# Kernel optimization log

Hardware: AMD Instinct MI355X
Metric: run time of the kernel (lower is better)

The kernel has to match this reference:

```python
import jax, jax.numpy as jnp
import numpy as np

CHUNK = 2048  # row tile size; keeps the [CHUNK, M] tile ~268 MB


def setup_inputs() -> dict:
    key = jax.random.key(0)
    k1, k2, k3 = jax.random.split(key, 3)
    N, M, D = 32768, 32768, 32
    ls = jax.random.uniform(k1, (1,), dtype=jnp.float32, minval=0.1, maxval=1.0)
    x = jax.random.normal(k2, (N, D), dtype=jnp.float32)
    y = jax.random.normal(k3, (M, D), dtype=jnp.float32)
    return {"ls": ls, "x": x, "y": y}


def reference(ls, x, y):
    # out[i] = sum_j exp(-ls * ||x_i - y_j||^2), computed in row tiles
    # (never materializes the full N x M matrix, like KeOps Genred).
    N, D = x.shape
    y_sq = jnp.sum(y * y, axis=1)  # [M]

    def row_chunk(xc):
        # xc: [CHUNK, D]
        x_sq = jnp.sum(xc * xc, axis=1)  # [CHUNK]
        sq = x_sq[:, None] + y_sq[None, :] - 2.0 * (xc @ y.T)  # [CHUNK, M]
        return jnp.sum(jnp.exp(-ls[0] * sq), axis=1)  # [CHUNK]

    x_tiles = x.reshape(N // CHUNK, CHUNK, D)
    out = jax.lax.map(row_chunk, x_tiles)  # [N//CHUNK, CHUNK]
    return out.reshape(N, 1)
```

## Files before the change

### kernel.cpp

```cpp
#include <hip/hip_runtime.h>
#include <math.h>

#define DIM 32
#define BLK 256
#define JSPLIT 16
#define RI   4
#define ITPB (4*RI)
#define GTT  16

typedef _Float16 half8 __attribute__((ext_vector_type(8)));
typedef float    f32x4 __attribute__((ext_vector_type(4)));
typedef float    f32x2 __attribute__((ext_vector_type(2)));

struct hl16 { half8 h; half8 l; };


__global__ __launch_bounds__(BLK) void rbf_prep(
    const float* __restrict__ lsp, const float* __restrict__ x,
    const float* __restrict__ y, int n, int m,
    double* __restrict__ acc, double* __restrict__ scale,
    float* __restrict__ bf, hl16* __restrict__ xhl, hl16* __restrict__ yhl)
{
    int i = blockIdx.x * BLK + threadIdx.x;
    const double c2 = -(double)lsp[0] * 1.4426950408889634074;
    const float mf = (float)(-2.0 * c2);
    if (i < n) {
        const float* xp = x + (size_t)i * DIM;
        double xs = 0.0;
        #pragma unroll
        for (int d = 0; d < DIM; ++d) { double v = (double)xp[d]; xs = fma(v, v, xs); }
        acc[i] = 0.0;
        scale[i] = exp2(c2 * xs);
        const int it = i >> 4, r15 = i & 15;
        #pragma unroll
        for (int q = 0; q < 4; ++q) {
            half8 hh, hl;
            #pragma unroll
            for (int d = 0; d < 8; ++d) {
                float v = xp[q * 8 + d] * mf;
                _Float16 h = (_Float16)v;
                hh[d] = h;
                hl[d] = (_Float16)((v - (float)h) * 4096.0f);
            }
            xhl[it * 64 + q * 16 + r15].h = hh;
            xhl[it * 64 + q * 16 + r15].l = hl;
        }
    }
    if (i < m) {
        const float* yp = y + (size_t)i * DIM;
        double ys = 0.0;
        #pragma unroll
        for (int d = 0; d < DIM; ++d) { double v = (double)yp[d]; ys = fma(v, v, ys); }
        bf[i] = (float)(c2 * ys);
        const int it = i >> 4, r15 = i & 15;
        #pragma unroll
        for (int q = 0; q < 4; ++q) {
            half8 hh, hl;
            #pragma unroll
            for (int d = 0; d < 8; ++d) {
                float v = yp[q * 8 + d];
                _Float16 h = (_Float16)v;
                hh[d] = h;
                hl[d] = (_Float16)((v - (float)h) * 4096.0f);
            }
            yhl[it * 64 + q * 16 + r15].h = hh;
            yhl[it * 64 + q * 16 + r15].l = hl;
        }
    }
}

__global__ __launch_bounds__(BLK, 4) void rbf_main(
    const hl16* __restrict__ xhl, const hl16* __restrict__ yhl,
    const float* __restrict__ bf, double* __restrict__ acc, int chunk_j)
{
    const int lane = threadIdx.x & 63;
    const int wave = threadIdx.x >> 6;
    const int itbase = blockIdx.x * ITPB + wave * RI;
    const int c15 = lane & 15;

    half8 ah[RI], al[RI];
    #pragma unroll
    for (int r = 0; r < RI; ++r) {
        ah[r] = xhl[(itbase + r) * 64 + lane].h;
        al[r] = xhl[(itbase + r) * 64 + lane].l;
    }

    const int jt0 = (blockIdx.y * chunk_j) >> 4;
    const int njt = chunk_j >> 4;

    const f32x4 zq = {0.0f, 0.0f, 0.0f, 0.0f};
    const float k12 = 0x1p-12f;

    double accd[RI][4];
    #pragma unroll
    for (int r = 0; r < RI; ++r)
        #pragma unroll
        for (int e = 0; e < 4; ++e) accd[r][e] = 0.0;

    half8 bh[2], bl[2];
    float bfv[2];
    bh[0] = yhl[(size_t)jt0 * 64 + lane].h;
    bl[0] = yhl[(size_t)jt0 * 64 + lane].l;
    bfv[0] = bf[jt0 * 16 + c15];

    for (int g = 0; g < njt / GTT; ++g) {
        f32x2 accf[RI][2];
        #pragma unroll
        for (int r = 0; r < RI; ++r) {
            accf[r][0] = (f32x2){0.0f, 0.0f};
            accf[r][1] = (f32x2){0.0f, 0.0f};
        }

        #pragma unroll
        for (int tt = 0; tt < GTT; ++tt) {
            const int cur = tt & 1, nxt = cur ^ 1;
            const int jt = jt0 + g * GTT + tt;
            int jn = jt + 1; if (jn >= jt0 + njt) jn = jt0;
            const hl16* __restrict__ yt = yhl + (size_t)jn * 64;
            bh[nxt] = yt[lane].h;
            bl[nxt] = yt[lane].l;
            bfv[nxt] = (bf + jn * 16)[c15];

            f32x2 bf2 = {bfv[cur], bfv[cur]};
            #pragma unroll
            for (int r = 0; r < RI; ++r) {
                f32x4 cm = __builtin_amdgcn_mfma_f32_16x16x32_f16(ah[r], bh[cur], zq, 0, 0, 0);
                f32x4 cl = __builtin_amdgcn_mfma_f32_16x16x32_f16(ah[r], bl[cur], zq, 0, 0, 0);
                cl = __builtin_amdgcn_mfma_f32_16x16x32_f16(al[r], bh[cur], cl, 0, 0, 0);
                f32x2 f0 = {cm[0], cm[1]}, f1 = {cm[2], cm[3]};
                f32x2 l0 = {cl[0], cl[1]}, l1 = {cl[2], cl[3]};
                f0 = l0 * k12 + f0;
                f1 = l1 * k12 + f1;
                f0 = f0 + bf2;
                f1 = f1 + bf2;
                f32x2 e0 = {__builtin_amdgcn_exp2f(f0.x), __builtin_amdgcn_exp2f(f0.y)};
                f32x2 e1 = {__builtin_amdgcn_exp2f(f1.x), __builtin_amdgcn_exp2f(f1.y)};
                accf[r][0] += e0;
                accf[r][1] += e1;
            }
        }
        #pragma unroll
        for (int r = 0; r < RI; ++r) {
            accd[r][0] += (double)accf[r][0].x;
            accd[r][1] += (double)accf[r][0].y;
            accd[r][2] += (double)accf[r][1].x;
            accd[r][3] += (double)accf[r][1].y;
        }
    }

    #pragma unroll
    for (int r = 0; r < RI; ++r) {
        #pragma unroll
        for (int e = 0; e < 4; ++e) {
            double v = accd[r][e];
            v += __shfl_xor(v, 1, 64);
            v += __shfl_xor(v, 2, 64);
            v += __shfl_xor(v, 4, 64);
            v += __shfl_xor(v, 8, 64);
            if (c15 == 0) {
                int row = (itbase + r) * 16 + (lane >> 4) * 4 + e;
                atomicAdd(&acc[row], v);
            }
        }
    }
}

__global__ __launch_bounds__(BLK) void rbf_finish(
    const double* __restrict__ acc, const double* __restrict__ scale,
    float* __restrict__ out, int n)
{
    int i = blockIdx.x * BLK + threadIdx.x;
    if (i < n) out[i] = (float)(acc[i] * scale[i]);
}

extern "C" void kernel_launch(void* const* d_in, const int* in_sizes, int n_in,
                              void* d_out, int out_size, void* d_ws, size_t ws_size,
                              hipStream_t stream)
{
    const float* ls = (const float*)d_in[0];
    const float* x  = (const float*)d_in[1];
    const float* y  = (const float*)d_in[2];
    const int n = in_sizes[1] / DIM;
    const int m = in_sizes[2] / DIM;
    float* out = (float*)d_out;

    char* ws = (char*)d_ws;
    double* acc   = (double*)ws;
    double* scale = acc + n;
    float*  bf    = (float*)(scale + n);
    hl16*   xhl   = (hl16*)(bf + m);
    hl16*   yhl   = xhl + (size_t)(n / 16) * 64;

    const int nm = (n > m) ? n : m;
    rbf_prep<<<(nm + BLK - 1) / BLK, BLK, 0, stream>>>(
        ls, x, y, n, m, acc, scale, bf, xhl, yhl);

    const int chunk = m / JSPLIT;
    dim3 grid(n / (16 * ITPB), JSPLIT);
    rbf_main<<<grid, BLK, 0, stream>>>(xhl, yhl, bf, acc, chunk);

    rbf_finish<<<(n + BLK - 1) / BLK, BLK, 0, stream>>>(acc, scale, out, n);
}
```

Before: 303.4 us.

## Replace hardware exp2 with packed polynomial exp2 and halve row tiles per wave

Computes exp2 in software: a magic-number round-to-integer, a degree-7 polynomial on the fractional part and exponent-bit construction, all in packed f32x2 arithmetic so it can use packed FMA instructions. The goal is to move work off the transcendental unit, which may be the throughput limit. It also reorders the bias addition and halves the row tiles per wave (RI 4 to 2), which doubles the grid and cuts register pressure. The trade-off is many more vector ALU instructions per element, plus fewer MFMA issues per B-tile load.

```diff
diff --git a/kernel.cpp b/kernel.cpp
--- a/kernel.cpp
+++ b/kernel.cpp
@@ -4,7 +4,7 @@
 #define DIM 32
 #define BLK 256
 #define JSPLIT 16
-#define RI   4
+#define RI   2
 #define ITPB (4*RI)
 #define GTT  16
 
@@ -69,6 +69,34 @@
     }
 }
 
+#define C7 1.5252733804059838e-05f
+#define C6 0.00015403530393381608f
+#define C5 0.0013333558146428443f
+#define C4 0.009618129107628477f
+#define C3 0.05550410866482158f
+#define C2f 0.2402265069591007f
+#define C1f 0.6931471805599453f
+#define KMAGIC 12582912.0f
+
+__device__ __forceinline__ void exp2_acc2(f32x2 f, f32x2& accv) {
+    f32x2 fc = { fmaxf(f.x, -126.0f), fmaxf(f.y, -126.0f) };
+    f32x2 t  = fc + (f32x2){KMAGIC, KMAGIC};
+    f32x2 nf = t - (f32x2){KMAGIC, KMAGIC};
+    f32x2 r  = fc - nf;
+    f32x2 p  = {C7, C7};
+    p = p * r + (f32x2){C6, C6};
+    p = p * r + (f32x2){C5, C5};
+    p = p * r + (f32x2){C4, C4};
+    p = p * r + (f32x2){C3, C3};
+    p = p * r + (f32x2){C2f, C2f};
+    p = p * r + (f32x2){C1f, C1f};
+    p = p * r + (f32x2){1.0f, 1.0f};
+    unsigned sx = (__float_as_uint(t.x) << 23) + 0x3F800000u;
+    unsigned sy = (__float_as_uint(t.y) << 23) + 0x3F800000u;
+    f32x2 s = { __uint_as_float(sx), __uint_as_float(sy) };
+    accv = p * s + accv;
+}
+
 __global__ __launch_bounds__(BLK, 4) void rbf_main(
     const hl16* __restrict__ xhl, const hl16* __restrict__ yhl,
     const float* __restrict__ bf, double* __restrict__ acc, int chunk_j)
@@ -129,14 +157,12 @@
                 cl = __builtin_amdgcn_mfma_f32_16x16x32_f16(al[r], bh[cur], cl, 0, 0, 0);
                 f32x2 f0 = {cm[0], cm[1]}, f1 = {cm[2], cm[3]};
                 f32x2 l0 = {cl[0], cl[1]}, l1 = {cl[2], cl[3]};
-                f0 = l0 * k12 + f0;
-                f1 = l1 * k12 + f1;
-                f0 = f0 + bf2;
-                f1 = f1 + bf2;
-                f32x2 e0 = {__builtin_amdgcn_exp2f(f0.x), __builtin_amdgcn_exp2f(f0.y)};
-                f32x2 e1 = {__builtin_amdgcn_exp2f(f1.x), __builtin_amdgcn_exp2f(f1.y)};
-                accf[r][0] += e0;
-                accf[r][1] += e1;
+                l0 = l0 * k12 + bf2;
+                l1 = l1 * k12 + bf2;
+                f0 = f0 + l0;
+                f1 = f1 + l1;
+                exp2_acc2(f0, accf[r][0]);
+                exp2_acc2(f1, accf[r][1]);
             }
         }
         #pragma unroll
```

After: 480.6 us. 1.58x slower.

## Fold bias into MFMA accumulator, halve rows per wave, simplify prefetch addressing

Applied to the files above, without the earlier changes.

Adds the y-norm bias to the low-part MFMA accumulator init (pre-scaled by 4096), so each output element needs only one FMA before exp2 and the separate bias add disappears. Cuts rows per wave from 4 to 2, which doubles the grid and lowers register pressure at the cost of reusing each y tile less. Prefetch addressing becomes a plain group-relative offset with no wraparound branch, so it reads one tile past the chunk. To keep that overread inside the workspace, yhl is moved before xhl. The bias folding also slightly changes the float rounding.

```diff
diff --git a/kernel.cpp b/kernel.cpp
--- a/kernel.cpp
+++ b/kernel.cpp
@@ -4,13 +4,12 @@
 #define DIM 32
 #define BLK 256
 #define JSPLIT 16
-#define RI   4
+#define RI   2
 #define ITPB (4*RI)
 #define GTT  16
 
 typedef _Float16 half8 __attribute__((ext_vector_type(8)));
 typedef float    f32x4 __attribute__((ext_vector_type(4)));
-typedef float    f32x2 __attribute__((ext_vector_type(2)));
 
 struct hl16 { half8 h; half8 l; };
 
@@ -104,48 +103,41 @@
     bfv[0] = bf[jt0 * 16 + c15];
 
     for (int g = 0; g < njt / GTT; ++g) {
-        f32x2 accf[RI][2];
+        const hl16*  __restrict__ ygrp = yhl + ((size_t)jt0 + (size_t)g * GTT) * 64;
+        const float* __restrict__ bgrp = bf + (jt0 + g * GTT) * 16;
+
+        float accf[RI][4];
         #pragma unroll
-        for (int r = 0; r < RI; ++r) {
-            accf[r][0] = (f32x2){0.0f, 0.0f};
-            accf[r][1] = (f32x2){0.0f, 0.0f};
-        }
+        for (int r = 0; r < RI; ++r)
+            #pragma unroll
+            for (int e = 0; e < 4; ++e) accf[r][e] = 0.0f;
 
         #pragma unroll
         for (int tt = 0; tt < GTT; ++tt) {
             const int cur = tt & 1, nxt = cur ^ 1;
-            const int jt = jt0 + g * GTT + tt;
-            int jn = jt + 1; if (jn >= jt0 + njt) jn = jt0;
-            const hl16* __restrict__ yt = yhl + (size_t)jn * 64;
-            bh[nxt] = yt[lane].h;
-            bl[nxt] = yt[lane].l;
-            bfv[nxt] = (bf + jn * 16)[c15];
+            bh[nxt] = ygrp[(tt + 1) * 64 + lane].h;
+            bl[nxt] = ygrp[(tt + 1) * 64 + lane].l;
+            bfv[nxt] = bgrp[(tt + 1) * 16 + c15];
 
-            f32x2 bf2 = {bfv[cur], bfv[cur]};
+            const float bq1 = bfv[cur] * 4096.0f;
+            const f32x4 bq = {bq1, bq1, bq1, bq1};
+
             #pragma unroll
             for (int r = 0; r < RI; ++r) {
                 f32x4 cm = __builtin_amdgcn_mfma_f32_16x16x32_f16(ah[r], bh[cur], zq, 0, 0, 0);
-                f32x4 cl = __builtin_amdgcn_mfma_f32_16x16x32_f16(ah[r], bl[cur], zq, 0, 0, 0);
-                cl = __builtin_amdgcn_mfma_f32_16x16x32_f16(al[r], bh[cur], cl, 0, 0, 0);
-                f32x2 f0 = {cm[0], cm[1]}, f1 = {cm[2], cm[3]};
-                f32x2 l0 = {cl[0], cl[1]}, l1 = {cl[2], cl[3]};
-                f0 = l0 * k12 + f0;
-                f1 = l1 * k12 + f1;
-                f0 = f0 + bf2;
-                f1 = f1 + bf2;
-                f32x2 e0 = {__builtin_amdgcn_exp2f(f0.x), __builtin_amdgcn_exp2f(f0.y)};
-                f32x2 e1 = {__builtin_amdgcn_exp2f(f1.x), __builtin_amdgcn_exp2f(f1.y)};
-                accf[r][0] += e0;
-                accf[r][1] += e1;
+                f32x4 cl = __builtin_amdgcn_mfma_f32_16x16x32_f16(al[r], bh[cur], bq, 0, 0, 0);
+                cl = __builtin_amdgcn_mfma_f32_16x16x32_f16(ah[r], bl[cur], cl, 0, 0, 0);
+                #pragma unroll
+                for (int e = 0; e < 4; ++e) {
+                    float f = __builtin_fmaf(cl[e], k12, cm[e]);
+                    accf[r][e] += __builtin_amdgcn_exp2f(f);
+                }
             }
         }
         #pragma unroll
-        for (int r = 0; r < RI; ++r) {
-            accd[r][0] += (double)accf[r][0].x;
-            accd[r][1] += (double)accf[r][0].y;
-            accd[r][2] += (double)accf[r][1].x;
-            accd[r][3] += (double)accf[r][1].y;
-        }
+        for (int r = 0; r < RI; ++r)
+            #pragma unroll
+            for (int e = 0; e < 4; ++e) accd[r][e] += (double)accf[r][e];
     }
 
     #pragma unroll
@@ -188,8 +180,8 @@
     double* acc   = (double*)ws;
     double* scale = acc + n;
     float*  bf    = (float*)(scale + n);
-    hl16*   xhl   = (hl16*)(bf + m);
-    hl16*   yhl   = xhl + (size_t)(n / 16) * 64;
+    hl16*   yhl   = (hl16*)(bf + m);
+    hl16*   xhl   = yhl + (size_t)(m / 16) * 64;
 
     const int nm = (n > m) ? n : m;
     rbf_prep<<<(nm + BLK - 1) / BLK, BLK, 0, stream>>>(
```

After: 304.3 us. About the same (+0.3%).
